# Optimization experiments

Measured on AMD Instinct MI355X. Metric: run time of the kernel, lower is better.

The kernel has to match this reference:

```python
import jax, jax.numpy as jnp
import numpy as np

G, P, D, K, H = 256, 1024, 128, 16, 32  # graphs, nodes/graph, feat dim, clusters, MLP hidden
N = G * P


def setup_inputs() -> dict:
    key = jax.random.key(0)
    k0, k1, k2 = jax.random.split(key, 3)
    node_feats = jax.random.normal(k0, (N, D), dtype=jnp.float32)
    W1 = jax.random.normal(k1, (D, H), dtype=jnp.float32) * (1.0 / np.sqrt(D))
    b1 = jnp.zeros((H,), dtype=jnp.float32)
    W2 = jax.random.normal(k2, (H, K), dtype=jnp.float32) * (1.0 / np.sqrt(H))
    b2 = jnp.zeros((K,), dtype=jnp.float32)
    n_node = jnp.full((G,), P, dtype=jnp.int32)
    return {"node_feats": node_feats, "W1": W1, "b1": b1, "W2": W2, "b2": b2, "n_node": n_node}


def reference(node_feats, W1, b1, W2, b2, n_node):
    num_nodes = node_feats.shape[0]
    num_graphs = n_node.shape[0]
    num_clusters = W2.shape[1]

    # MLP([32, K]) assignment logits + softmax
    h = jax.nn.relu(node_feats @ W1 + b1)
    assignments = jax.nn.softmax(h @ W2 + b2, axis=-1)  # [N, K]

    # graph id per node
    batch_indices = jnp.repeat(jnp.arange(num_graphs), n_node, total_repeat_length=num_nodes)

    # per-cluster weighted segment_sum (loop over small fixed K, as in the original)
    coarse = [
        jax.ops.segment_sum(node_feats * assignments[:, k:k + 1], batch_indices, num_segments=num_graphs)
        for k in range(num_clusters)
    ]
    coarse_nodes = jnp.stack(coarse, axis=1).reshape(-1, node_feats.shape[-1])  # [G*K, D]

    # fully-connected coarse edges per graph (nonzero of ones is row-major: sender repeated, receiver tiled)
    single_senders = jnp.repeat(jnp.arange(num_clusters), num_clusters)
    single_receivers = jnp.tile(jnp.arange(num_clusters), num_clusters)
    batch_offset = jnp.arange(num_graphs)[:, None] * num_clusters
    c_senders = (single_senders[None, :] + batch_offset).reshape(-1)
    c_receivers = (single_receivers[None, :] + batch_offset).reshape(-1)
    c_edges = jnp.ones((c_senders.shape[0], 1), dtype=node_feats.dtype)

    return coarse_nodes, assignments, c_senders, c_receivers, c_edges
```

## Files before the change

kernel.cpp:

```cpp
#include <hip/hip_runtime.h>
#include <hip/hip_bf16.h>
#include <cstdint>

#define G_ 256
#define P_ 1024
#define D_ 128
#define K_ 16
#define H_ 32
#define N_ (G_ * P_)

constexpr size_t OFF_COARSE = 0;
constexpr size_t OFF_ASSIGN = (size_t)G_ * K_ * D_;
constexpr size_t OFF_SEND   = OFF_ASSIGN + (size_t)N_ * K_;
constexpr size_t OFF_RECV   = OFF_SEND + (size_t)G_ * K_ * K_;
constexpr size_t OFF_EDGE   = OFF_RECV + (size_t)G_ * K_ * K_;

typedef __attribute__((ext_vector_type(8))) short bf16x8;
typedef __attribute__((ext_vector_type(4))) float f32x4;

__device__ __forceinline__ unsigned rpack(float a, float b) {
    const unsigned ua = __float_as_uint(a) + 0x8000u;
    const unsigned ub = __float_as_uint(b) + 0x8000u;
    return (ua >> 16) | (ub & 0xffff0000u);
}
__device__ __forceinline__ short rbf16(float a) {
    return (short)((__float_as_uint(a) + 0x8000u) >> 16);
}

union FragU { uint4 u; bf16x8 v; };

__global__ __launch_bounds__(256, 4) void mlp_assign_mfma(
    const float* __restrict__ x, const float* __restrict__ W1,
    const float* __restrict__ b1, const float* __restrict__ W2,
    const float* __restrict__ b2, float* __restrict__ assign_out)
{
    __shared__ short    w1s[4096];
    __shared__ unsigned hstage[4][512];

    const int tid  = threadIdx.x;
    const int lane = tid & 63;
    const int wave = tid >> 6;
    const int q = lane >> 4;
    const int c = lane & 15;

    for (int i = tid; i < 4096; i += 256) {
        const int e  = i & 7;
        const int cc = (i >> 3) & 15;
        const int qq = (i >> 7) & 3;
        const int nt = (i >> 9) & 1;
        const int kb = (i >> 10) & 3;
        w1s[(((kb * 2 + nt) * 4 + qq) * 16 + cc) * 8 + e] =
            rbf16(W1[(kb * 32 + qq * 8 + e) * H_ + nt * 16 + cc]);
    }
    __syncthreads();

    FragU w2f;
    {
        float wv[8];
#pragma unroll
        for (int e = 0; e < 8; ++e) wv[e] = W2[(q * 8 + e) * K_ + c];
        w2f.u = make_uint4(rpack(wv[0], wv[1]), rpack(wv[2], wv[3]),
                           rpack(wv[4], wv[5]), rpack(wv[6], wv[7]));
    }
    const float b1v0 = b1[c];
    const float b1v1 = b1[16 + c];
    const float b2v  = b2[c];

    unsigned* hw = hstage[wave];
    const size_t nodebase = (size_t)blockIdx.x * 256 + (size_t)wave * 64;

    float4 ld[8];
    {
        const float* rp = x + (nodebase + c) * D_ + q * 8;
#pragma unroll
        for (int kb = 0; kb < 4; ++kb) {
            ld[kb * 2 + 0] = *(const float4*)(rp + kb * 32);
            ld[kb * 2 + 1] = *(const float4*)(rp + kb * 32 + 4);
        }
    }

#pragma unroll
    for (int mt = 0; mt < 4; ++mt) {
        FragU af[4];
#pragma unroll
        for (int kb = 0; kb < 4; ++kb) {
            const float4 v0 = ld[kb * 2 + 0];
            const float4 v1 = ld[kb * 2 + 1];
            af[kb].u = make_uint4(rpack(v0.x, v0.y), rpack(v0.z, v0.w),
                                  rpack(v1.x, v1.y), rpack(v1.z, v1.w));
        }
        if (mt < 3) {
            const float* rp = x + (nodebase + (size_t)(mt + 1) * 16 + c) * D_ + q * 8;
#pragma unroll
            for (int kb = 0; kb < 4; ++kb) {
                ld[kb * 2 + 0] = *(const float4*)(rp + kb * 32);
                ld[kb * 2 + 1] = *(const float4*)(rp + kb * 32 + 4);
            }
        }

        f32x4 acc0 = {b1v0, b1v0, b1v0, b1v0};
        f32x4 acc1 = {b1v1, b1v1, b1v1, b1v1};
#pragma unroll
        for (int kb = 0; kb < 4; ++kb) {
            const bf16x8 bh0 = *(const bf16x8*)&w1s[((kb * 2 + 0) * 4 + q) * 128 + c * 8];
            const bf16x8 bh1 = *(const bf16x8*)&w1s[((kb * 2 + 1) * 4 + q) * 128 + c * 8];
            acc0 = __builtin_amdgcn_mfma_f32_16x16x32_bf16(af[kb].v, bh0, acc0, 0, 0, 0);
            acc1 = __builtin_amdgcn_mfma_f32_16x16x32_bf16(af[kb].v, bh1, acc1, 0, 0, 0);
        }

#pragma unroll
        for (int r = 0; r < 4; ++r) {
            const int row = q * 4 + r;
            const int xsw = (row & 7) << 2;
            hw[(row * 32 + c) ^ xsw] =
                (unsigned)(unsigned short)rbf16(fmaxf(acc0[r], 0.f));
            hw[(row * 32 + 16 + c) ^ xsw] =
                (unsigned)(unsigned short)rbf16(fmaxf(acc1[r], 0.f));
        }

        const int hsw = (c & 7) << 2;
        const uint4 u0 = *(const uint4*)&hw[(c * 32 + q * 8) ^ hsw];
        const uint4 u1 = *(const uint4*)&hw[(c * 32 + q * 8 + 4) ^ hsw];
        FragU ha;
        ha.u.x = (u0.x & 0xffffu) | (u0.y << 16);
        ha.u.y = (u0.z & 0xffffu) | (u0.w << 16);
        ha.u.z = (u1.x & 0xffffu) | (u1.y << 16);
        ha.u.w = (u1.z & 0xffffu) | (u1.w << 16);

        f32x4 lacc = {b2v, b2v, b2v, b2v};
        lacc = __builtin_amdgcn_mfma_f32_16x16x32_bf16(ha.v, w2f.v, lacc, 0, 0, 0);

        float ex0 = __expf(lacc[0]);
        float ex1 = __expf(lacc[1]);
        float ex2 = __expf(lacc[2]);
        float ex3 = __expf(lacc[3]);
        float s0 = ex0, s1 = ex1, s2 = ex2, s3 = ex3;
#pragma unroll
        for (int s = 1; s < 16; s <<= 1) {
            s0 += __shfl_xor(s0, s, 16);
            s1 += __shfl_xor(s1, s, 16);
            s2 += __shfl_xor(s2, s, 16);
            s3 += __shfl_xor(s3, s, 16);
        }
        const size_t ob = (nodebase + (size_t)mt * 16 + q * 4) * K_ + c;
        assign_out[ob + 0 * K_] = ex0 / s0;
        assign_out[ob + 1 * K_] = ex1 / s1;
        assign_out[ob + 2 * K_] = ex2 / s2;
        assign_out[ob + 3 * K_] = ex3 / s3;
    }
}

#define FMA4(dst, v, sc)                                                      \
    dst.x = fmaf(v.x, sc, dst.x); dst.y = fmaf(v.y, sc, dst.y);               \
    dst.z = fmaf(v.z, sc, dst.z); dst.w = fmaf(v.w, sc, dst.w)

__global__ __launch_bounds__(1024, 4) void coarse_kernel(
    const float* __restrict__ x, const float* __restrict__ assign,
    const int* __restrict__ n_node, float* __restrict__ out)
{
    __shared__ float xs[2][32 * 128];
    __shared__ float as_[2][32 * 16];
    __shared__ int pref[G_];

    const int tid = threadIdx.x;
    const int g = blockIdx.x;

    if (tid < 256) {
        const int e = g * 256 + tid;
        out[OFF_SEND + e] = (float)(g * K_ + (tid >> 4));
        out[OFF_RECV + e] = (float)(g * K_ + (tid & 15));
        out[OFF_EDGE + e] = 1.0f;
    }

    if (tid < G_) pref[tid] = n_node[tid];
    __syncthreads();
    for (int st = 1; st < G_; st <<= 1) {
        int v = 0;
        if (tid < G_ && tid >= st) v = pref[tid - st];
        __syncthreads();
        if (tid < G_ && tid >= st) pref[tid] += v;
        __syncthreads();
    }
    const int start = (g == 0) ? 0 : min(pref[g - 1], N_);
    const int end   = (g == G_ - 1) ? N_ : min(pref[g], N_);

    const int dq = tid & 31;
    const int s  = tid >> 5;

    float4 acc[K_];
#pragma unroll
    for (int k = 0; k < K_; ++k) acc[k] = make_float4(0.f, 0.f, 0.f, 0.f);

    const int total = end - start;
    const int nfull = total >> 5;
    const int tail  = total & 31;

    float4 rx = make_float4(0.f, 0.f, 0.f, 0.f);
    float4 ra = make_float4(0.f, 0.f, 0.f, 0.f);
    if (nfull > 0) {
        rx = *(const float4*)(x + (size_t)start * D_ + tid * 4);
        if (tid < 128)
            ra = *(const float4*)(assign + (size_t)start * K_ + tid * 4);
    }

    int b = 0;
    for (int cc = 0; cc < nfull; ++cc) {
        *(float4*)(&xs[b][tid * 4]) = rx;
        if (tid < 128) *(float4*)(&as_[b][tid * 4]) = ra;
        __syncthreads();

        if (cc + 1 < nfull) {
            const size_t nb = (size_t)start + (size_t)(cc + 1) * 32;
            rx = *(const float4*)(x + nb * D_ + tid * 4);
            if (tid < 128)
                ra = *(const float4*)(assign + nb * K_ + tid * 4);
        }

        const float4 xv = *(const float4*)(&xs[b][s * D_ + dq * 4]);
        const float4* av = (const float4*)(&as_[b][s * K_]);
#pragma unroll
        for (int qq = 0; qq < 4; ++qq) {
            const float4 a = av[qq];
            FMA4(acc[4 * qq + 0], xv, a.x);
            FMA4(acc[4 * qq + 1], xv, a.y);
            FMA4(acc[4 * qq + 2], xv, a.z);
            FMA4(acc[4 * qq + 3], xv, a.w);
        }
        b ^= 1;
    }

    if (tail > 0 && s < tail) {
        const size_t n = (size_t)start + (size_t)nfull * 32 + s;
        const float4 xv = *(const float4*)(x + n * D_ + dq * 4);
        const float4* av = (const float4*)(assign + n * K_);
#pragma unroll
        for (int qq = 0; qq < 4; ++qq) {
            const float4 a = av[qq];
            FMA4(acc[4 * qq + 0], xv, a.x);
            FMA4(acc[4 * qq + 1], xv, a.y);
            FMA4(acc[4 * qq + 2], xv, a.z);
            FMA4(acc[4 * qq + 3], xv, a.w);
        }
    }

    __syncthreads();
    float* red = &xs[0][0];
#pragma unroll
    for (int k = 0; k < K_; ++k) {
        *(float4*)(&red[s * D_ + dq * 4]) = acc[k];
        __syncthreads();
        if (tid < D_) {
            float sum = 0.f;
#pragma unroll
            for (int ss = 0; ss < 32; ++ss) sum += red[ss * D_ + tid];
            out[OFF_COARSE + ((size_t)g * K_ + k) * D_ + tid] = sum;
        }
        __syncthreads();
    }
}

extern "C" void kernel_launch(void* const* d_in, const int* in_sizes, int n_in,
                              void* d_out, int out_size, void* d_ws, size_t ws_size,
                              hipStream_t stream)
{
    const float* x      = (const float*)d_in[0];
    const float* W1     = (const float*)d_in[1];
    const float* b1     = (const float*)d_in[2];
    const float* W2     = (const float*)d_in[3];
    const float* b2     = (const float*)d_in[4];
    const int*   n_node = (const int*)d_in[5];
    float* out = (float*)d_out;

    mlp_assign_mfma<<<N_ / 256, 256, 0, stream>>>(x, W1, b1, W2, b2, out + OFF_ASSIGN);
    coarse_kernel<<<G_, 1024, 0, stream>>>(x, out + OFF_ASSIGN, n_node, out);
}
```

Measured before the change: 64.84 us.

## Stage node features through swizzled LDS with coalesced block-wide loads in MLP kernel

The MLP assignment kernel now loads each 64-node tile of features with fully coalesced float4 reads across the whole block into a 32 KB XOR-swizzled LDS buffer. Waves then read their MFMA A-fragments from LDS instead of doing strided per-lane global loads. The next tile's global load is issued before compute, and the node-to-wave mapping changes so each wave handles 16 nodes per tile. This adds two block barriers per tile and more LDS usage, with occupancy lowered from 4 to 3 blocks per CU.

```diff
diff --git a/kernel.cpp b/kernel.cpp
--- a/kernel.cpp
+++ b/kernel.cpp
@@ -29,11 +29,12 @@
 
 union FragU { uint4 u; bf16x8 v; };
 
-__global__ __launch_bounds__(256, 4) void mlp_assign_mfma(
+__global__ __launch_bounds__(256, 3) void mlp_assign_mfma(
     const float* __restrict__ x, const float* __restrict__ W1,
     const float* __restrict__ b1, const float* __restrict__ W2,
     const float* __restrict__ b2, float* __restrict__ assign_out)
 {
+    __shared__ float    xstage[4 * 16 * 128];
     __shared__ short    w1s[4096];
     __shared__ unsigned hstage[4][512];
 
@@ -42,6 +43,8 @@
     const int wave = tid >> 6;
     const int q = lane >> 4;
     const int c = lane & 15;
+
+    const size_t blockbase = (size_t)blockIdx.x * 256;
 
     for (int i = tid; i < 4096; i += 256) {
         const int e  = i & 7;
@@ -52,7 +55,6 @@
         w1s[(((kb * 2 + nt) * 4 + qq) * 16 + cc) * 8 + e] =
             rbf16(W1[(kb * 32 + qq * 8 + e) * H_ + nt * 16 + cc]);
     }
-    __syncthreads();
 
     FragU w2f;
     {
@@ -65,37 +67,48 @@
     const float b1v0 = b1[c];
     const float b1v1 = b1[16 + c];
     const float b2v  = b2[c];
-
     unsigned* hw = hstage[wave];
-    const size_t nodebase = (size_t)blockIdx.x * 256 + (size_t)wave * 64;
+
+    int sbyte[8];
+#pragma unroll
+    for (int i = 0; i < 8; ++i) {
+        const int v = i * 256 + tid;
+        const int row64 = v >> 5;
+        const int slot  = v & 31;
+        sbyte[i] = (row64 >> 4) * 8192 +
+                   ((((row64 & 15) * 512) + slot * 16) ^ ((row64 & 7) << 4));
+    }
 
     float4 ld[8];
     {
-        const float* rp = x + (nodebase + c) * D_ + q * 8;
+        const float4* src = (const float4*)(x + blockbase * D_);
+#pragma unroll
+        for (int i = 0; i < 8; ++i) ld[i] = src[i * 256 + tid];
+#pragma unroll
+        for (int i = 0; i < 8; ++i)
+            *(float4*)((char*)xstage + sbyte[i]) = ld[i];
+    }
+    __syncthreads();
+
+    const int fragbase = wave * 8192;
+    const int csw = (c & 7) << 4;
+
+#pragma unroll 1
+    for (int t = 0; t < 4; ++t) {
+        if (t < 3) {
+            const float4* src = (const float4*)(x + (blockbase + (size_t)(t + 1) * 64) * D_);
+#pragma unroll
+            for (int i = 0; i < 8; ++i) ld[i] = src[i * 256 + tid];
+        }
+
+        FragU af[4];
 #pragma unroll
         for (int kb = 0; kb < 4; ++kb) {
-            ld[kb * 2 + 0] = *(const float4*)(rp + kb * 32);
-            ld[kb * 2 + 1] = *(const float4*)(rp + kb * 32 + 4);
-        }
-    }
-
-#pragma unroll
-    for (int mt = 0; mt < 4; ++mt) {
-        FragU af[4];
-#pragma unroll
-        for (int kb = 0; kb < 4; ++kb) {
-            const float4 v0 = ld[kb * 2 + 0];
-            const float4 v1 = ld[kb * 2 + 1];
+            const int p0 = c * 512 + kb * 128 + q * 32;
+            const float4 v0 = *(const float4*)((char*)xstage + fragbase + (p0 ^ csw));
+            const float4 v1 = *(const float4*)((char*)xstage + fragbase + ((p0 + 16) ^ csw));
             af[kb].u = make_uint4(rpack(v0.x, v0.y), rpack(v0.z, v0.w),
                                   rpack(v1.x, v1.y), rpack(v1.z, v1.w));
-        }
-        if (mt < 3) {
-            const float* rp = x + (nodebase + (size_t)(mt + 1) * 16 + c) * D_ + q * 8;
-#pragma unroll
-            for (int kb = 0; kb < 4; ++kb) {
-                ld[kb * 2 + 0] = *(const float4*)(rp + kb * 32);
-                ld[kb * 2 + 1] = *(const float4*)(rp + kb * 32 + 4);
-            }
         }
 
         f32x4 acc0 = {b1v0, b1v0, b1v0, b1v0};
@@ -142,11 +155,20 @@
             s2 += __shfl_xor(s2, s, 16);
             s3 += __shfl_xor(s3, s, 16);
         }
-        const size_t ob = (nodebase + (size_t)mt * 16 + q * 4) * K_ + c;
+        const size_t node0 = blockbase + (size_t)t * 64 + (size_t)wave * 16 + q * 4;
+        const size_t ob = node0 * K_ + c;
         assign_out[ob + 0 * K_] = ex0 / s0;
         assign_out[ob + 1 * K_] = ex1 / s1;
         assign_out[ob + 2 * K_] = ex2 / s2;
         assign_out[ob + 3 * K_] = ex3 / s3;
+
+        __syncthreads();
+        if (t < 3) {
+#pragma unroll
+            for (int i = 0; i < 8; ++i)
+                *(float4*)((char*)xstage + sbyte[i]) = ld[i];
+        }
+        __syncthreads();
     }
 }
 
```

Result: slower. 87.77 us (+35.4%).
